# Optimization experiments

Measured on AMD Instinct MI355X. Metric: run time of the kernel, lower is better.

## Reference

```python
import jax, jax.numpy as jnp
import numpy as np

N = 116                      # AAL atlas nodes
E = N * (N - 1) // 2         # 6670 edges of the fully connected connectome
HID = 64
EDIM = 5
OUT = 4
ENC = HID + N // 2           # 122 raw brain-encoding features
EPS = 1e-10


def setup_inputs() -> dict:
    key = jax.random.key(0)
    ks = jax.random.split(key, 15)
    iu = np.triu_indices(N, k=1)                      # matches torch.nonzero(triu) order
    edge_index = jnp.asarray(np.stack(iu), dtype=jnp.int32)   # [2, E]
    rn = lambda k, s, sc=0.1: jax.random.normal(k, s, dtype=jnp.float32) * sc
    return dict(
        encoding_raw=rn(ks[0], (N, ENC), 1.0),
        edge_attr=rn(ks[1], (E, EDIM), 1.0),
        edge_index=edge_index,
        W_enc=rn(ks[2], (ENC, HID)), b_enc=rn(ks[3], (HID,)),
        W1=rn(ks[4], (HID, HID)), b1=rn(ks[5], (HID,)), p1=rn(ks[6], (1, EDIM)),
        We=rn(ks[7], (EDIM, EDIM)), be=rn(ks[8], (EDIM,)), pe=rn(ks[9], (1, HID)),
        W2=rn(ks[10], (HID, HID)), b2=rn(ks[11], (HID,)), p2=rn(ks[12], (1, EDIM)),
        Wl=rn(ks[13], (HID, OUT)), bl=rn(ks[14], (OUT,)),
    )


def _forward(encoding_raw, edge_attr, edge_index, W_enc, b_enc,
             W1, b1, p1, We, be, pe, W2, b2, p2, Wl, bl):
    eye_n = jnp.eye(N, dtype=jnp.float32)
    eye_e = jnp.eye(E, dtype=jnp.float32)
    adj_v = 1.0 - eye_n          # fully-connected node adjacency, zero diagonal
    adj_e = 1.0 - eye_e          # edge adjacency: ones minus eye
    # Incidence matrix T [N, E]: T[i,e] = T[j,e] = 1 for edge e = (i, j)
    cols = jnp.arange(E)
    T = (jnp.zeros((N, E), dtype=jnp.float32)
         .at[edge_index[0], cols].set(1.0)
         .at[edge_index[1], cols].set(1.0))

    # BrainEncoding: x = Linear(raw encoding)  (batch.x is None -> x = encodings)
    x = encoding_raw @ W_enc + b_enc                    # [N, HID]

    def node_conv(Hv, He, W, b, p):
        d = (He @ p.T)[:, 0]                            # [E] learned scalar per edge
        mult = (T * d) @ T.T                            # T diag(d) T^T  -> [N, N]
        # M1 = eye*1 + (1-eye)*mult, then * adj_v (zero diag) => mult * adj_v
        A = mult * adj_v
        return A @ (Hv @ W) + b

    def edge_conv(Hv, He, W, b, p):
        dv = (Hv @ p.T)[:, 0]                           # [N] learned scalar per node
        mult = T.T @ (dv[:, None] * T)                  # T^T diag(dv) T -> [E, E] dense
        A = mult * adj_e                                # M3 * adj_e => zero diag, off-diag mult
        A = A / (A.max(axis=0, keepdims=True) + EPS)    # column-max normalization
        return A @ (He @ W) + b

    # node_conv1 -> relu (dropout is identity in eval)
    x = jax.nn.relu(node_conv(x, edge_attr, W1, b1, p1))
    e = jax.nn.relu(edge_attr)
    # edge_conv1 -> relu
    e = jax.nn.relu(edge_conv(x, e, We, be, pe))
    x = jax.nn.relu(x)                                  # relu applied again (idempotent)
    # node_conv2 (no relu after)
    x = node_conv(x, e, W2, b2, p2)
    # global mean pool over the single graph, then classifier head
    pooled = jnp.mean(x, axis=0, keepdims=True)         # [1, HID]
    return pooled @ Wl + bl                             # [1, OUT]


def reference(encoding_raw, edge_attr, edge_index, W_enc, b_enc,
              W1, b1, p1, We, be, pe, W2, b2, p2, Wl, bl):
    return _forward(encoding_raw, edge_attr, edge_index, W_enc, b_enc,
                    W1, b1, p1, We, be, pe, W2, b2, p2, Wl, bl)
```

## Files before the change

### kernel.cpp

```cpp
#include <hip/hip_runtime.h>


#define NN   116
#define EE   6670
#define HID  64
#define EDIM 5
#define OUTD 4
#define ENC  122
#define EPSF 1e-10f
#define NH   (NN*HID)

__device__ __forceinline__ int eid_ij(int i, int j) {
    int a = i < j ? i : j;
    int b = i < j ? j : i;
    return a*NN - ((a*(a+1)) >> 1) + (b - a - 1);
}

__global__ __launch_bounds__(256) void kA(
    const float* __restrict__ enc, const float* __restrict__ ea,
    const float* __restrict__ W_enc, const float* __restrict__ b_enc,
    const float* __restrict__ p1, const float* __restrict__ We,
    const float* __restrict__ W1,
    float* __restrict__ Y1, float* __restrict__ d1, float* __restrict__ G)
{
    const int tid = threadIdx.x;
    if (blockIdx.x < 29) {
        __shared__ __align__(16) float sWe[ENC*HID];
        __shared__ __align__(16) float sW1[HID*HID];
        __shared__ __align__(16) float sEnc[4*ENC];
        __shared__ float sX[4*HID];
        {
            const float4* g4 = (const float4*)W_enc; float4* s4 = (float4*)sWe;
            for (int u = tid; u < ENC*HID/4; u += 256) s4[u] = g4[u];
        }
        {
            const float4* g4 = (const float4*)W1; float4* s4 = (float4*)sW1;
            for (int u = tid; u < HID*HID/4; u += 256) s4[u] = g4[u];
        }
        {
            const float4* g4 = (const float4*)(enc + blockIdx.x*4*ENC);
            float4* s4 = (float4*)sEnc;
            for (int u = tid; u < 4*ENC/4; u += 256) s4[u] = g4[u];
        }
        __syncthreads();
        const int w = tid >> 6, h = tid & 63;
        const int i = blockIdx.x*4 + w;
        float acc = b_enc[h];
        const float* er = sEnc + w*ENC;
        #pragma unroll 4
        for (int k = 0; k < ENC; ++k) acc = fmaf(er[k], sWe[k*HID + h], acc);
        sX[w*HID + h] = acc;
        __syncthreads();
        float a2 = 0.f;
        const float* xr = sX + w*HID;
        #pragma unroll 8
        for (int k = 0; k < HID; ++k) a2 = fmaf(xr[k], sW1[k*HID + h], a2);
        Y1[i*HID + h] = a2;
    } else {
        int u = (blockIdx.x - 29)*256 + tid;
        if (u < EE) {
            const float* r = ea + u*EDIM;
            float a0 = 0.f;
            #pragma unroll
            for (int k = 0; k < EDIM; ++k) a0 = fmaf(r[k], p1[k], a0);
            d1[u] = a0;
        } else if (u < EE + EE*EDIM) {
            int idx = u - EE;
            int e = idx / EDIM, k = idx - e*EDIM;
            const float* r = ea + e*EDIM;
            float a0 = 0.f;
            #pragma unroll
            for (int m = 0; m < EDIM; ++m) a0 = fmaf(fmaxf(r[m], 0.f), We[m*EDIM + k], a0);
            G[idx] = a0;
        }
    }
}

__global__ __launch_bounds__(256) void kB(
    const float* __restrict__ d1, const float* __restrict__ Y1,
    const float* __restrict__ b1, const float* __restrict__ pe,
    const float* __restrict__ W2,
    float* __restrict__ dv, float* __restrict__ Y2)
{
    __shared__ __align__(16) float sY[NH];
    __shared__ __align__(16) float sD[EE];
    __shared__ float sX2[4*HID];
    const int tid = threadIdx.x;
    {
        const float4* g4 = (const float4*)Y1; float4* s4 = (float4*)sY;
        for (int u = tid; u < NH/4; u += 256) s4[u] = g4[u];
        const float2* g2 = (const float2*)d1; float2* s2 = (float2*)sD;
        for (int u = tid; u < EE/2; u += 256) s2[u] = g2[u];
    }
    __syncthreads();
    const int w = tid >> 6, h = tid & 63;
    const int i = blockIdx.x*4 + w;
    float acc = b1[h];
    #pragma unroll 4
    for (int j = 0; j < NN; ++j) {
        int jj = (j == i) ? (j ^ 1) : j;
        float wgt = (j == i) ? 0.f : sD[eid_ij(i, jj)];
        acc = fmaf(wgt, sY[jj*HID + h], acc);
    }
    float v = fmaxf(acc, 0.f);
    float r = v * pe[h];
    #pragma unroll
    for (int off = 32; off > 0; off >>= 1) r += __shfl_down(r, off, 64);
    if (h == 0) dv[i] = r;
    sX2[w*HID + h] = v;
    __syncthreads();
    float a2 = 0.f;
    const float* xr = sX2 + w*HID;
    #pragma unroll 8
    for (int k = 0; k < HID; ++k) a2 = fmaf(xr[k], W2[k*HID + h], a2);
    Y2[i*HID + h] = a2;
}

__global__ __launch_bounds__(256) void kC(
    const float* __restrict__ G, const float* __restrict__ dv,
    float* __restrict__ S)
{
    const int wg = blockIdx.x*4 + (threadIdx.x >> 6);
    const int lane = threadIdx.x & 63;
    const int i = wg / EDIM, k = wg - i*EDIM;
    const float di = dv[i];
    float acc = 0.f;
    #pragma unroll
    for (int rep = 0; rep < 2; ++rep) {
        int j = lane + rep*64;
        if (j < NN && j != i) {
            float cm = fmaxf(fmaxf(di, dv[j]), 0.f) + EPSF;
            acc += G[eid_ij(i, j)*EDIM + k] / cm;
        }
    }
    #pragma unroll
    for (int off = 32; off > 0; off >>= 1) acc += __shfl_down(acc, off, 64);
    if (lane == 0) S[wg] = acc;
}

__global__ __launch_bounds__(256) void kD(
    const int* __restrict__ eidx, const float* __restrict__ G,
    const float* __restrict__ dv, const float* __restrict__ S,
    const float* __restrict__ be, const float* __restrict__ p2,
    float* __restrict__ d2, float* __restrict__ P)
{
    const int t = blockIdx.x*256 + threadIdx.x;
    if (blockIdx.x == 0 && threadIdx.x < HID) P[threadIdx.x] = 0.f;
    if (t >= EE) return;
    const int a = eidx[t], b = eidx[EE + t];
    const float da = dv[a], db = dv[b];
    const float rc = 1.f / (fmaxf(fmaxf(da, db), 0.f) + EPSF);
    float acc = 0.f;
    #pragma unroll
    for (int kk = 0; kk < EDIM; ++kk) {
        float gp = G[t*EDIM + kk] * rc;
        float v = fmaf(da, S[a*EDIM + kk] - gp, fmaf(db, S[b*EDIM + kk] - gp, be[kk]));
        acc = fmaf(fmaxf(v, 0.f), p2[kk], acc);
    }
    d2[t] = acc;
}

__global__ __launch_bounds__(256) void kE(
    const float* __restrict__ d2, const float* __restrict__ Y2,
    const float* __restrict__ b2, float* __restrict__ P)
{
    __shared__ __align__(16) float sY[NH];
    __shared__ __align__(16) float sD[EE];
    __shared__ float sR[4*HID];
    const int tid = threadIdx.x;
    {
        const float4* g4 = (const float4*)Y2; float4* s4 = (float4*)sY;
        for (int u = tid; u < NH/4; u += 256) s4[u] = g4[u];
        const float2* g2 = (const float2*)d2; float2* s2 = (float2*)sD;
        for (int u = tid; u < EE/2; u += 256) s2[u] = g2[u];
    }
    __syncthreads();
    const int w = tid >> 6, h = tid & 63;
    const int i = blockIdx.x*4 + w;
    float acc = b2[h];
    #pragma unroll 4
    for (int j = 0; j < NN; ++j) {
        int jj = (j == i) ? (j ^ 1) : j;
        float wgt = (j == i) ? 0.f : sD[eid_ij(i, jj)];
        acc = fmaf(wgt, sY[jj*HID + h], acc);
    }
    sR[w*HID + h] = acc;
    __syncthreads();
    if (w == 0) {
        float s4 = sR[h] + sR[HID + h] + sR[2*HID + h] + sR[3*HID + h];
        atomicAdd(&P[h], s4);
    }
}

__global__ void kF(const float* __restrict__ P, const float* __restrict__ Wl,
                   const float* __restrict__ bl, float* __restrict__ out)
{
    const int lane = threadIdx.x;
    float val = P[lane] * (1.0f / NN);
    float res[OUTD];
    #pragma unroll
    for (int o = 0; o < OUTD; ++o) {
        float r = val * Wl[lane*OUTD + o];
        #pragma unroll
        for (int off = 32; off > 0; off >>= 1) r += __shfl_xor(r, off, 64);
        res[o] = r;
    }
    if (lane < OUTD) out[lane] = res[lane] + bl[lane];
}

extern "C" void kernel_launch(void* const* d_in, const int* in_sizes, int n_in,
                              void* d_out, int out_size, void* d_ws, size_t ws_size,
                              hipStream_t stream)
{
    const float* enc   = (const float*)d_in[0];
    const float* ea    = (const float*)d_in[1];
    const int*   eidx  = (const int*)  d_in[2];
    const float* W_enc = (const float*)d_in[3];
    const float* b_enc = (const float*)d_in[4];
    const float* W1    = (const float*)d_in[5];
    const float* b1    = (const float*)d_in[6];
    const float* p1    = (const float*)d_in[7];
    const float* We    = (const float*)d_in[8];
    const float* be    = (const float*)d_in[9];
    const float* pe    = (const float*)d_in[10];
    const float* W2    = (const float*)d_in[11];
    const float* b2    = (const float*)d_in[12];
    const float* p2    = (const float*)d_in[13];
    const float* Wl    = (const float*)d_in[14];
    const float* bl    = (const float*)d_in[15];
    float* ws = (float*)d_ws;

    float* Y1 = ws;
    float* P  = ws;
    float* Y2 = ws + NH;
    float* dA = ws + 2*NH;
    float* G  = dA + EE;
    float* dv = G + EE*EDIM;
    float* S  = dv + NN;
    float* out = (float*)d_out;

    kA<<<29 + (EE + EE*EDIM + 255)/256, 256, 0, stream>>>(enc, ea, W_enc, b_enc, p1, We, W1, Y1, dA, G);
    kB<<<29, 256, 0, stream>>>(dA, Y1, b1, pe, W2, dv, Y2);
    kC<<<(NN*EDIM)/4, 256, 0, stream>>>(G, dv, S);
    kD<<<(EE + 255)/256, 256, 0, stream>>>(eidx, G, dv, S, be, p2, dA, P);
    kE<<<29, 256, 0, stream>>>(dA, Y2, b2, P);
    kF<<<1, 64, 0, stream>>>(P, Wl, bl, out);
}
```

Measured before the change: 126.3 us.

## Fuse six kernels into one cooperative kernel with grid-wide syncs

```diff
diff --git a/kernel.cpp b/kernel.cpp
--- a/kernel.cpp
+++ b/kernel.cpp
@@ -1,4 +1,7 @@
 #include <hip/hip_runtime.h>
+#include <hip/hip_cooperative_groups.h>
+
+namespace cg = cooperative_groups;
 
 
 #define NN   116
@@ -9,6 +12,7 @@
 #define ENC  122
 #define EPSF 1e-10f
 #define NH   (NN*HID)
+#define GB   64
 
 __device__ __forceinline__ int eid_ij(int i, int j) {
     int a = i < j ? i : j;
@@ -16,19 +20,38 @@
     return a*NN - ((a*(a+1)) >> 1) + (b - a - 1);
 }
 
-__global__ __launch_bounds__(256) void kA(
+__global__ __launch_bounds__(256) void fused(
     const float* __restrict__ enc, const float* __restrict__ ea,
+    const int* __restrict__ eidx,
     const float* __restrict__ W_enc, const float* __restrict__ b_enc,
+    const float* __restrict__ W1, const float* __restrict__ b1,
     const float* __restrict__ p1, const float* __restrict__ We,
-    const float* __restrict__ W1,
-    float* __restrict__ Y1, float* __restrict__ d1, float* __restrict__ G)
+    const float* __restrict__ be, const float* __restrict__ pe,
+    const float* __restrict__ W2, const float* __restrict__ b2,
+    const float* __restrict__ p2, const float* __restrict__ Wl,
+    const float* __restrict__ bl,
+    float* __restrict__ ws, float* __restrict__ out)
 {
+    __shared__ __align__(16) float smem[14352];
+    cg::grid_group grid = cg::this_grid();
     const int tid = threadIdx.x;
-    if (blockIdx.x < 29) {
-        __shared__ __align__(16) float sWe[ENC*HID];
-        __shared__ __align__(16) float sW1[HID*HID];
-        __shared__ __align__(16) float sEnc[4*ENC];
-        __shared__ float sX[4*HID];
+    const int bid = blockIdx.x;
+    const int w = tid >> 6, h = tid & 63;
+
+    float* Y1 = ws;
+    float* Y2 = ws + NH;
+    float* d1 = ws + 2*NH;
+    float* G  = d1 + EE;
+    float* dv = G + EE*EDIM;
+    float* S  = dv + NN;
+    float* d2 = S + NN*EDIM;
+    float* P  = d2 + EE;
+
+    if (bid < 29) {
+        float* sWe  = smem;
+        float* sW1  = smem + 7808;
+        float* sEnc = smem + 11904;
+        float* sX   = smem + 12392;
         {
             const float4* g4 = (const float4*)W_enc; float4* s4 = (float4*)sWe;
             for (int u = tid; u < ENC*HID/4; u += 256) s4[u] = g4[u];
@@ -38,13 +61,12 @@
             for (int u = tid; u < HID*HID/4; u += 256) s4[u] = g4[u];
         }
         {
-            const float4* g4 = (const float4*)(enc + blockIdx.x*4*ENC);
+            const float4* g4 = (const float4*)(enc + bid*4*ENC);
             float4* s4 = (float4*)sEnc;
             for (int u = tid; u < 4*ENC/4; u += 256) s4[u] = g4[u];
         }
         __syncthreads();
-        const int w = tid >> 6, h = tid & 63;
-        const int i = blockIdx.x*4 + w;
+        const int i = bid*4 + w;
         float acc = b_enc[h];
         const float* er = sEnc + w*ENC;
         #pragma unroll 4
@@ -57,155 +79,134 @@
         for (int k = 0; k < HID; ++k) a2 = fmaf(xr[k], sW1[k*HID + h], a2);
         Y1[i*HID + h] = a2;
     } else {
-        int u = (blockIdx.x - 29)*256 + tid;
-        if (u < EE) {
-            const float* r = ea + u*EDIM;
-            float a0 = 0.f;
+        for (int u = (bid - 29)*256 + tid; u < EE + EE*EDIM; u += (GB - 29)*256) {
+            if (u < EE) {
+                const float* r = ea + u*EDIM;
+                float a0 = 0.f;
+                #pragma unroll
+                for (int k = 0; k < EDIM; ++k) a0 = fmaf(r[k], p1[k], a0);
+                d1[u] = a0;
+            } else {
+                int idx = u - EE;
+                int e = idx / EDIM, k = idx - e*EDIM;
+                const float* r = ea + e*EDIM;
+                float a0 = 0.f;
+                #pragma unroll
+                for (int m = 0; m < EDIM; ++m) a0 = fmaf(fmaxf(r[m], 0.f), We[m*EDIM + k], a0);
+                G[idx] = a0;
+            }
+        }
+    }
+    grid.sync();
+
+    if (bid < 29) {
+        float* sY  = smem;
+        float* sD  = smem + NH;
+        float* sX2 = smem + 14094;
+        {
+            const float4* g4 = (const float4*)Y1; float4* s4 = (float4*)sY;
+            for (int u = tid; u < NH/4; u += 256) s4[u] = g4[u];
+            const float2* g2 = (const float2*)d1; float2* s2 = (float2*)sD;
+            for (int u = tid; u < EE/2; u += 256) s2[u] = g2[u];
+        }
+        __syncthreads();
+        const int i = bid*4 + w;
+        float acc = b1[h];
+        #pragma unroll 4
+        for (int j = 0; j < NN; ++j) {
+            int jj = (j == i) ? (j ^ 1) : j;
+            float wgt = (j == i) ? 0.f : sD[eid_ij(i, jj)];
+            acc = fmaf(wgt, sY[jj*HID + h], acc);
+        }
+        float v = fmaxf(acc, 0.f);
+        float r = v * pe[h];
+        #pragma unroll
+        for (int off = 32; off > 0; off >>= 1) r += __shfl_down(r, off, 64);
+        if (h == 0) dv[i] = r;
+        sX2[w*HID + h] = v;
+        __syncthreads();
+        float a2 = 0.f;
+        const float* xr = sX2 + w*HID;
+        #pragma unroll 8
+        for (int k = 0; k < HID; ++k) a2 = fmaf(xr[k], W2[k*HID + h], a2);
+        Y2[i*HID + h] = a2;
+    }
+    grid.sync();
+
+    for (int wg = bid*4 + w; wg < NN*EDIM; wg += GB*4) {
+        const int i = wg / EDIM, k = wg - i*EDIM;
+        const float di = dv[i];
+        float acc = 0.f;
+        #pragma unroll
+        for (int rep = 0; rep < 2; ++rep) {
+            int j = h + rep*64;
+            if (j < NN && j != i) {
+                float cm = fmaxf(fmaxf(di, dv[j]), 0.f) + EPSF;
+                acc += G[eid_ij(i, j)*EDIM + k] / cm;
+            }
+        }
+        #pragma unroll
+        for (int off = 32; off > 0; off >>= 1) acc += __shfl_down(acc, off, 64);
+        if (h == 0) S[wg] = acc;
+    }
+    grid.sync();
+
+    if (bid == 0 && tid < HID) P[tid] = 0.f;
+    for (int t = bid*256 + tid; t < EE; t += GB*256) {
+        const int a = eidx[t], b = eidx[EE + t];
+        const float da = dv[a], db = dv[b];
+        const float rc = 1.f / (fmaxf(fmaxf(da, db), 0.f) + EPSF);
+        float acc = 0.f;
+        #pragma unroll
+        for (int kk = 0; kk < EDIM; ++kk) {
+            float gp = G[t*EDIM + kk] * rc;
+            float v = fmaf(da, S[a*EDIM + kk] - gp, fmaf(db, S[b*EDIM + kk] - gp, be[kk]));
+            acc = fmaf(fmaxf(v, 0.f), p2[kk], acc);
+        }
+        d2[t] = acc;
+    }
+    grid.sync();
+
+    if (bid < 29) {
+        float* sY = smem;
+        float* sD = smem + NH;
+        float* sR = smem + 14094;
+        {
+            const float4* g4 = (const float4*)Y2; float4* s4 = (float4*)sY;
+            for (int u = tid; u < NH/4; u += 256) s4[u] = g4[u];
+            const float2* g2 = (const float2*)d2; float2* s2 = (float2*)sD;
+            for (int u = tid; u < EE/2; u += 256) s2[u] = g2[u];
+        }
+        __syncthreads();
+        const int i = bid*4 + w;
+        float acc = b2[h];
+        #pragma unroll 4
+        for (int j = 0; j < NN; ++j) {
+            int jj = (j == i) ? (j ^ 1) : j;
+            float wgt = (j == i) ? 0.f : sD[eid_ij(i, jj)];
+            acc = fmaf(wgt, sY[jj*HID + h], acc);
+        }
+        sR[w*HID + h] = acc;
+        __syncthreads();
+        if (w == 0) {
+            float s4 = sR[h] + sR[HID + h] + sR[2*HID + h] + sR[3*HID + h];
+            atomicAdd(&P[h], s4);
+        }
+    }
+    grid.sync();
+
+    if (bid == 0 && tid < 64) {
+        float val = P[tid] * (1.0f / NN);
+        float res[OUTD];
+        #pragma unroll
+        for (int o = 0; o < OUTD; ++o) {
+            float r = val * Wl[tid*OUTD + o];
             #pragma unroll
-            for (int k = 0; k < EDIM; ++k) a0 = fmaf(r[k], p1[k], a0);
-            d1[u] = a0;
-        } else if (u < EE + EE*EDIM) {
-            int idx = u - EE;
-            int e = idx / EDIM, k = idx - e*EDIM;
-            const float* r = ea + e*EDIM;
-            float a0 = 0.f;
-            #pragma unroll
-            for (int m = 0; m < EDIM; ++m) a0 = fmaf(fmaxf(r[m], 0.f), We[m*EDIM + k], a0);
-            G[idx] = a0;
-        }
-    }
-}
-
-__global__ __launch_bounds__(256) void kB(
-    const float* __restrict__ d1, const float* __restrict__ Y1,
-    const float* __restrict__ b1, const float* __restrict__ pe,
-    const float* __restrict__ W2,
-    float* __restrict__ dv, float* __restrict__ Y2)
-{
-    __shared__ __align__(16) float sY[NH];
-    __shared__ __align__(16) float sD[EE];
-    __shared__ float sX2[4*HID];
-    const int tid = threadIdx.x;
-    {
-        const float4* g4 = (const float4*)Y1; float4* s4 = (float4*)sY;
-        for (int u = tid; u < NH/4; u += 256) s4[u] = g4[u];
-        const float2* g2 = (const float2*)d1; float2* s2 = (float2*)sD;
-        for (int u = tid; u < EE/2; u += 256) s2[u] = g2[u];
-    }
-    __syncthreads();
-    const int w = tid >> 6, h = tid & 63;
-    const int i = blockIdx.x*4 + w;
-    float acc = b1[h];
-    #pragma unroll 4
-    for (int j = 0; j < NN; ++j) {
-        int jj = (j == i) ? (j ^ 1) : j;
-        float wgt = (j == i) ? 0.f : sD[eid_ij(i, jj)];
-        acc = fmaf(wgt, sY[jj*HID + h], acc);
-    }
-    float v = fmaxf(acc, 0.f);
-    float r = v * pe[h];
-    #pragma unroll
-    for (int off = 32; off > 0; off >>= 1) r += __shfl_down(r, off, 64);
-    if (h == 0) dv[i] = r;
-    sX2[w*HID + h] = v;
-    __syncthreads();
-    float a2 = 0.f;
-    const float* xr = sX2 + w*HID;
-    #pragma unroll 8
-    for (int k = 0; k < HID; ++k) a2 = fmaf(xr[k], W2[k*HID + h], a2);
-    Y2[i*HID + h] = a2;
-}
-
-__global__ __launch_bounds__(256) void kC(
-    const float* __restrict__ G, const float* __restrict__ dv,
-    float* __restrict__ S)
-{
-    const int wg = blockIdx.x*4 + (threadIdx.x >> 6);
-    const int lane = threadIdx.x & 63;
-    const int i = wg / EDIM, k = wg - i*EDIM;
-    const float di = dv[i];
-    float acc = 0.f;
-    #pragma unroll
-    for (int rep = 0; rep < 2; ++rep) {
-        int j = lane + rep*64;
-        if (j < NN && j != i) {
-            float cm = fmaxf(fmaxf(di, dv[j]), 0.f) + EPSF;
-            acc += G[eid_ij(i, j)*EDIM + k] / cm;
-        }
-    }
-    #pragma unroll
-    for (int off = 32; off > 0; off >>= 1) acc += __shfl_down(acc, off, 64);
-    if (lane == 0) S[wg] = acc;
-}
-
-__global__ __launch_bounds__(256) void kD(
-    const int* __restrict__ eidx, const float* __restrict__ G,
-    const float* __restrict__ dv, const float* __restrict__ S,
-    const float* __restrict__ be, const float* __restrict__ p2,
-    float* __restrict__ d2, float* __restrict__ P)
-{
-    const int t = blockIdx.x*256 + threadIdx.x;
-    if (blockIdx.x == 0 && threadIdx.x < HID) P[threadIdx.x] = 0.f;
-    if (t >= EE) return;
-    const int a = eidx[t], b = eidx[EE + t];
-    const float da = dv[a], db = dv[b];
-    const float rc = 1.f / (fmaxf(fmaxf(da, db), 0.f) + EPSF);
-    float acc = 0.f;
-    #pragma unroll
-    for (int kk = 0; kk < EDIM; ++kk) {
-        float gp = G[t*EDIM + kk] * rc;
-        float v = fmaf(da, S[a*EDIM + kk] - gp, fmaf(db, S[b*EDIM + kk] - gp, be[kk]));
-        acc = fmaf(fmaxf(v, 0.f), p2[kk], acc);
-    }
-    d2[t] = acc;
-}
-
-__global__ __launch_bounds__(256) void kE(
-    const float* __restrict__ d2, const float* __restrict__ Y2,
-    const float* __restrict__ b2, float* __restrict__ P)
-{
-    __shared__ __align__(16) float sY[NH];
-    __shared__ __align__(16) float sD[EE];
-    __shared__ float sR[4*HID];
-    const int tid = threadIdx.x;
-    {
-        const float4* g4 = (const float4*)Y2; float4* s4 = (float4*)sY;
-        for (int u = tid; u < NH/4; u += 256) s4[u] = g4[u];
-        const float2* g2 = (const float2*)d2; float2* s2 = (float2*)sD;
-        for (int u = tid; u < EE/2; u += 256) s2[u] = g2[u];
-    }
-    __syncthreads();
-    const int w = tid >> 6, h = tid & 63;
-    const int i = blockIdx.x*4 + w;
-    float acc = b2[h];
-    #pragma unroll 4
-    for (int j = 0; j < NN; ++j) {
-        int jj = (j == i) ? (j ^ 1) : j;
-        float wgt = (j == i) ? 0.f : sD[eid_ij(i, jj)];
-        acc = fmaf(wgt, sY[jj*HID + h], acc);
-    }
-    sR[w*HID + h] = acc;
-    __syncthreads();
-    if (w == 0) {
-        float s4 = sR[h] + sR[HID + h] + sR[2*HID + h] + sR[3*HID + h];
-        atomicAdd(&P[h], s4);
-    }
-}
-
-__global__ void kF(const float* __restrict__ P, const float* __restrict__ Wl,
-                   const float* __restrict__ bl, float* __restrict__ out)
-{
-    const int lane = threadIdx.x;
-    float val = P[lane] * (1.0f / NN);
-    float res[OUTD];
-    #pragma unroll
-    for (int o = 0; o < OUTD; ++o) {
-        float r = val * Wl[lane*OUTD + o];
-        #pragma unroll
-        for (int off = 32; off > 0; off >>= 1) r += __shfl_xor(r, off, 64);
-        res[o] = r;
-    }
-    if (lane < OUTD) out[lane] = res[lane] + bl[lane];
+            for (int off = 32; off > 0; off >>= 1) r += __shfl_xor(r, off, 64);
+            res[o] = r;
+        }
+        if (tid < OUTD) out[tid] = res[tid] + bl[tid];
+    }
 }
 
 extern "C" void kernel_launch(void* const* d_in, const int* in_sizes, int n_in,
@@ -228,21 +229,14 @@
     const float* p2    = (const float*)d_in[13];
     const float* Wl    = (const float*)d_in[14];
     const float* bl    = (const float*)d_in[15];
-    float* ws = (float*)d_ws;
-
-    float* Y1 = ws;
-    float* P  = ws;
-    float* Y2 = ws + NH;
-    float* dA = ws + 2*NH;
-    float* G  = dA + EE;
-    float* dv = G + EE*EDIM;
-    float* S  = dv + NN;
+    float* ws  = (float*)d_ws;
     float* out = (float*)d_out;
 
-    kA<<<29 + (EE + EE*EDIM + 255)/256, 256, 0, stream>>>(enc, ea, W_enc, b_enc, p1, We, W1, Y1, dA, G);
-    kB<<<29, 256, 0, stream>>>(dA, Y1, b1, pe, W2, dv, Y2);
-    kC<<<(NN*EDIM)/4, 256, 0, stream>>>(G, dv, S);
-    kD<<<(EE + 255)/256, 256, 0, stream>>>(eidx, G, dv, S, be, p2, dA, P);
-    kE<<<29, 256, 0, stream>>>(dA, Y2, b2, P);
-    kF<<<1, 64, 0, stream>>>(P, Wl, bl, out);
+    void* args[] = {
+        (void*)&enc, (void*)&ea, (void*)&eidx, (void*)&W_enc, (void*)&b_enc,
+        (void*)&W1, (void*)&b1, (void*)&p1, (void*)&We, (void*)&be, (void*)&pe,
+        (void*)&W2, (void*)&b2, (void*)&p2, (void*)&Wl, (void*)&bl,
+        (void*)&ws, (void*)&out
+    };
+    hipLaunchCooperativeKernel((void*)fused, dim3(GB), dim3(256), args, 0, stream);
 }
```

New measurement: 188.0 us. 48.8% more time.

## Fuse edge conv, node conv2 and head into one kernel with redundant S

Applied to the files above, without the earlier changes.

```diff
diff --git a/kernel.cpp b/kernel.cpp
--- a/kernel.cpp
+++ b/kernel.cpp
@@ -9,6 +9,7 @@
 #define ENC  122
 #define EPSF 1e-10f
 #define NH   (NN*HID)
+#define CH   27
 
 __device__ __forceinline__ int eid_ij(int i, int j) {
     int a = i < j ? i : j;
@@ -80,12 +81,17 @@
     const float* __restrict__ d1, const float* __restrict__ Y1,
     const float* __restrict__ b1, const float* __restrict__ pe,
     const float* __restrict__ W2,
-    float* __restrict__ dv, float* __restrict__ Y2)
+    float* __restrict__ dv, float* __restrict__ Y2,
+    float* __restrict__ P, int* __restrict__ cnt)
 {
     __shared__ __align__(16) float sY[NH];
     __shared__ __align__(16) float sD[EE];
     __shared__ float sX2[4*HID];
     const int tid = threadIdx.x;
+    if (blockIdx.x == 0) {
+        if (tid < HID) P[tid] = 0.f;
+        if (tid == 0) *cnt = 0;
+    }
     {
         const float4* g4 = (const float4*)Y1; float4* s4 = (float4*)sY;
         for (int u = tid; u < NH/4; u += 256) s4[u] = g4[u];
@@ -116,96 +122,110 @@
     Y2[i*HID + h] = a2;
 }
 
-__global__ __launch_bounds__(256) void kC(
-    const float* __restrict__ G, const float* __restrict__ dv,
-    float* __restrict__ S)
-{
-    const int wg = blockIdx.x*4 + (threadIdx.x >> 6);
-    const int lane = threadIdx.x & 63;
-    const int i = wg / EDIM, k = wg - i*EDIM;
-    const float di = dv[i];
-    float acc = 0.f;
-    #pragma unroll
-    for (int rep = 0; rep < 2; ++rep) {
-        int j = lane + rep*64;
-        if (j < NN && j != i) {
-            float cm = fmaxf(fmaxf(di, dv[j]), 0.f) + EPSF;
-            acc += G[eid_ij(i, j)*EDIM + k] / cm;
-        }
-    }
-    #pragma unroll
-    for (int off = 32; off > 0; off >>= 1) acc += __shfl_down(acc, off, 64);
-    if (lane == 0) S[wg] = acc;
-}
-
-__global__ __launch_bounds__(256) void kD(
+__global__ __launch_bounds__(256) void kCDEF(
     const int* __restrict__ eidx, const float* __restrict__ G,
-    const float* __restrict__ dv, const float* __restrict__ S,
+    const float* __restrict__ dvg, const float* __restrict__ Y2,
     const float* __restrict__ be, const float* __restrict__ p2,
-    float* __restrict__ d2, float* __restrict__ P)
-{
-    const int t = blockIdx.x*256 + threadIdx.x;
-    if (blockIdx.x == 0 && threadIdx.x < HID) P[threadIdx.x] = 0.f;
-    if (t >= EE) return;
-    const int a = eidx[t], b = eidx[EE + t];
-    const float da = dv[a], db = dv[b];
-    const float rc = 1.f / (fmaxf(fmaxf(da, db), 0.f) + EPSF);
-    float acc = 0.f;
-    #pragma unroll
-    for (int kk = 0; kk < EDIM; ++kk) {
-        float gp = G[t*EDIM + kk] * rc;
-        float v = fmaf(da, S[a*EDIM + kk] - gp, fmaf(db, S[b*EDIM + kk] - gp, be[kk]));
-        acc = fmaf(fmaxf(v, 0.f), p2[kk], acc);
-    }
-    d2[t] = acc;
-}
-
-__global__ __launch_bounds__(256) void kE(
-    const float* __restrict__ d2, const float* __restrict__ Y2,
-    const float* __restrict__ b2, float* __restrict__ P)
+    const float* __restrict__ b2, const float* __restrict__ Wl,
+    const float* __restrict__ bl,
+    float* __restrict__ P, int* __restrict__ cnt, float* __restrict__ out)
 {
     __shared__ __align__(16) float sY[NH];
-    __shared__ __align__(16) float sD[EE];
+    __shared__ float sS[NN*EDIM];
+    __shared__ float sDv[NN];
+    __shared__ float sD2[4*NN];
     __shared__ float sR[4*HID];
+    __shared__ int sLast;
     const int tid = threadIdx.x;
+    const int wid = tid >> 6, lane = tid & 63;
+
     {
         const float4* g4 = (const float4*)Y2; float4* s4 = (float4*)sY;
         for (int u = tid; u < NH/4; u += 256) s4[u] = g4[u];
-        const float2* g2 = (const float2*)d2; float2* s2 = (float2*)sD;
-        for (int u = tid; u < EE/2; u += 256) s2[u] = g2[u];
-    }
-    __syncthreads();
-    const int w = tid >> 6, h = tid & 63;
-    const int i = blockIdx.x*4 + w;
-    float acc = b2[h];
-    #pragma unroll 4
-    for (int j = 0; j < NN; ++j) {
-        int jj = (j == i) ? (j ^ 1) : j;
-        float wgt = (j == i) ? 0.f : sD[eid_ij(i, jj)];
-        acc = fmaf(wgt, sY[jj*HID + h], acc);
-    }
-    sR[w*HID + h] = acc;
-    __syncthreads();
-    if (w == 0) {
-        float s4 = sR[h] + sR[HID + h] + sR[2*HID + h] + sR[3*HID + h];
-        atomicAdd(&P[h], s4);
-    }
-}
-
-__global__ void kF(const float* __restrict__ P, const float* __restrict__ Wl,
-                   const float* __restrict__ bl, float* __restrict__ out)
-{
-    const int lane = threadIdx.x;
-    float val = P[lane] * (1.0f / NN);
-    float res[OUTD];
-    #pragma unroll
-    for (int o = 0; o < OUTD; ++o) {
-        float r = val * Wl[lane*OUTD + o];
+    }
+    if (tid < NN) sDv[tid] = dvg[tid];
+    for (int u = tid; u < NN*EDIM; u += 256) sS[u] = 0.f;
+    __syncthreads();
+
+    {
+        const int t0 = tid * CH;
+        const int t1 = (t0 + CH < EE) ? t0 + CH : EE;
+        for (int t = t0; t < t1; ++t) {
+            const int a = eidx[t], b = eidx[EE + t];
+            const float rc = 1.f / (fmaxf(fmaxf(sDv[a], sDv[b]), 0.f) + EPSF);
+            #pragma unroll
+            for (int k = 0; k < EDIM; ++k) {
+                const float gp = G[t*EDIM + k] * rc;
+                atomicAdd(&sS[a*EDIM + k], gp);
+                atomicAdd(&sS[b*EDIM + k], gp);
+            }
+        }
+    }
+    __syncthreads();
+
+    {
+        const int i = blockIdx.x*4 + wid;
+        float ber[EDIM], p2r[EDIM];
         #pragma unroll
-        for (int off = 32; off > 0; off >>= 1) r += __shfl_xor(r, off, 64);
-        res[o] = r;
-    }
-    if (lane < OUTD) out[lane] = res[lane] + bl[lane];
+        for (int k = 0; k < EDIM; ++k) { ber[k] = be[k]; p2r[k] = p2[k]; }
+        #pragma unroll
+        for (int rep = 0; rep < 2; ++rep) {
+            const int j = lane + rep*64;
+            if (j < NN) {
+                float val = 0.f;
+                if (j != i) {
+                    const int a = i < j ? i : j, b = i < j ? j : i;
+                    const int e = a*NN - ((a*(a+1)) >> 1) + (b - a - 1);
+                    const float da = sDv[a], db = sDv[b];
+                    const float rc = 1.f / (fmaxf(fmaxf(da, db), 0.f) + EPSF);
+                    #pragma unroll
+                    for (int k = 0; k < EDIM; ++k) {
+                        const float gp = G[e*EDIM + k] * rc;
+                        const float v = fmaf(da, sS[a*EDIM + k] - gp,
+                                       fmaf(db, sS[b*EDIM + k] - gp, ber[k]));
+                        val = fmaf(fmaxf(v, 0.f), p2r[k], val);
+                    }
+                }
+                sD2[wid*NN + j] = val;
+            }
+        }
+    }
+    __syncthreads();
+
+    {
+        float acc = b2[lane];
+        const float* d2r = sD2 + wid*NN;
+        #pragma unroll 4
+        for (int j = 0; j < NN; ++j)
+            acc = fmaf(d2r[j], sY[j*HID + lane], acc);
+        sR[wid*HID + lane] = acc;
+    }
+    __syncthreads();
+    if (wid == 0) {
+        float s4 = sR[lane] + sR[HID + lane] + sR[2*HID + lane] + sR[3*HID + lane];
+        atomicAdd(&P[lane], s4);
+    }
+    __syncthreads();
+
+    if (tid == 0) {
+        __threadfence();
+        int old = __hip_atomic_fetch_add(cnt, 1, __ATOMIC_ACQ_REL, __HIP_MEMORY_SCOPE_AGENT);
+        sLast = (old == 28) ? 1 : 0;
+    }
+    __syncthreads();
+    if (sLast && wid == 0) {
+        const float pv = __hip_atomic_load(&P[lane], __ATOMIC_ACQUIRE, __HIP_MEMORY_SCOPE_AGENT);
+        const float val = pv * (1.0f / NN);
+        float res[OUTD];
+        #pragma unroll
+        for (int o = 0; o < OUTD; ++o) {
+            float r = val * Wl[lane*OUTD + o];
+            #pragma unroll
+            for (int off = 32; off > 0; off >>= 1) r += __shfl_xor(r, off, 64);
+            res[o] = r;
+        }
+        if (lane < OUTD) out[lane] = res[lane] + bl[lane];
+    }
 }
 
 extern "C" void kernel_launch(void* const* d_in, const int* in_sizes, int n_in,
@@ -231,18 +251,15 @@
     float* ws = (float*)d_ws;
 
     float* Y1 = ws;
-    float* P  = ws;
     float* Y2 = ws + NH;
-    float* dA = ws + 2*NH;
-    float* G  = dA + EE;
+    float* d1 = ws + 2*NH;
+    float* G  = d1 + EE;
     float* dv = G + EE*EDIM;
-    float* S  = dv + NN;
+    float* P  = dv + NN;
+    int*  cnt = (int*)(P + HID);
     float* out = (float*)d_out;
 
-    kA<<<29 + (EE + EE*EDIM + 255)/256, 256, 0, stream>>>(enc, ea, W_enc, b_enc, p1, We, W1, Y1, dA, G);
-    kB<<<29, 256, 0, stream>>>(dA, Y1, b1, pe, W2, dv, Y2);
-    kC<<<(NN*EDIM)/4, 256, 0, stream>>>(G, dv, S);
-    kD<<<(EE + 255)/256, 256, 0, stream>>>(eidx, G, dv, S, be, p2, dA, P);
-    kE<<<29, 256, 0, stream>>>(dA, Y2, b2, P);
-    kF<<<1, 64, 0, stream>>>(P, Wl, bl, out);
-}
+    kA<<<29 + (EE + EE*EDIM + 255)/256, 256, 0, stream>>>(enc, ea, W_enc, b_enc, p1, We, W1, Y1, d1, G);
+    kB<<<29, 256, 0, stream>>>(d1, Y1, b1, pe, W2, dv, Y2, P, cnt);
+    kCDEF<<<29, 256, 0, stream>>>(eidx, G, dv, Y2, be, p2, b2, Wl, bl, P, cnt, out);
+}
```

New measurement: 204.7 us. +62.1%, slower.
